# Kernel tuning notes

Hardware: AMD Instinct MI355X
Metric: run time of the kernel (lower is better)

The kernel has to match this reference:

```python
import jax, jax.numpy as jnp
import numpy as np

EPS = 0.0  # GINConv eps

def _gin_conv(x, edge_index, W1, b1, W2, b2, n_nodes):
    # GINConv: mlp((1+eps)*x + sum_{j in N(i)} x_j)
    src, dst = edge_index[0], edge_index[1]
    agg = jax.ops.segment_sum(x[src], dst, num_segments=n_nodes)  # [N, d]
    h = (1.0 + EPS) * x + agg
    h = jax.nn.relu(h @ W1 + b1)  # Linear -> Identity(BN off) -> ReLU
    return h @ W2 + b2            # second Linear


def setup_inputs() -> dict:
    key = jax.random.key(0)
    ks = jax.random.split(key, 10)
    N, E = 50000, 600000
    d_in, d_hid, d_out = 128, 256, 128
    x = jax.random.normal(ks[0], (N, d_in), dtype=jnp.float32)
    edge_index = jax.random.randint(ks[1], (2, E), 0, N, dtype=jnp.int64)

    def lin(k, fan_in, fan_out):
        bound = 1.0 / np.sqrt(fan_in)
        kw, kb = jax.random.split(k)
        W = jax.random.uniform(kw, (fan_in, fan_out), jnp.float32, -bound, bound)
        b = jax.random.uniform(kb, (fan_out,), jnp.float32, -bound, bound)
        return W, b

    W1a, b1a = lin(ks[2], d_in, d_hid)   # conv0 mlp: 128->256
    W2a, b2a = lin(ks[3], d_hid, d_hid)  # conv0 mlp: 256->256
    W1b, b1b = lin(ks[4], d_hid, d_hid)  # conv1 mlp: 256->256
    W2b, b2b = lin(ks[5], d_hid, d_out)  # conv1 mlp: 256->128
    return {"x": x, "W1a": W1a, "b1a": b1a, "W2a": W2a, "b2a": b2a,
            "W1b": W1b, "b1b": b1b, "W2b": W2b, "b2b": b2b,
            "edge_index": edge_index}


def reference(x, W1a, b1a, W2a, b2a, W1b, b1b, W2b, b2b, edge_index):
    n_nodes = x.shape[0]
    # layer 0: GINConv -> relu (use_bn=False; dropout is identity in eval)
    h = _gin_conv(x, edge_index, W1a, b1a, W2a, b2a, n_nodes)
    h = jax.nn.relu(h)
    # final GINConv (no activation after, per forward())
    return _gin_conv(h, edge_index, W1b, b1b, W2b, b2b, n_nodes)
```

## Files before the change

kernel.cpp:

```cpp
#include <hip/hip_runtime.h>


typedef __bf16 bf16x8 __attribute__((ext_vector_type(8)));
typedef float f32x4 __attribute__((ext_vector_type(4)));
typedef float f32x2 __attribute__((ext_vector_type(2)));
typedef unsigned short u16x4 __attribute__((ext_vector_type(4)));
typedef unsigned short u16x8 __attribute__((ext_vector_type(8)));
typedef unsigned int uint32;
typedef uint32 u32x4 __attribute__((ext_vector_type(4)));

__device__ __forceinline__ unsigned short f2bf(float f) {
  uint32 u = __builtin_bit_cast(uint32, f);
  u += 0x7FFFu + ((u >> 16) & 1u);
  return (unsigned short)(u >> 16);
}
__device__ __forceinline__ f32x2 bfpair(uint32 w) {
  f32x2 r;
  r.x = __builtin_bit_cast(float, w << 16);
  r.y = __builtin_bit_cast(float, w & 0xFFFF0000u);
  return r;
}

#define G2L16(gp, lp)                                                        \
  __builtin_amdgcn_global_load_lds(                                          \
      (const __attribute__((address_space(1))) void*)(gp),                   \
      (__attribute__((address_space(3))) void*)(lp), 16, 0, 0)

__global__ void hist(const int* __restrict__ eidx, int* __restrict__ deg, int E) {
  int e = blockIdx.x * blockDim.x + threadIdx.x;
  if (e < E) atomicAdd(&deg[eidx[e + E]], 1);
}

__global__ __launch_bounds__(256) void scan_all(
    const int* __restrict__ deg, int* __restrict__ offs, int* __restrict__ pos,
    int* __restrict__ aggr, int* __restrict__ incl, int* __restrict__ flg,
    int Nn, int nb) {
  __shared__ int sm[256];
  __shared__ int s_prefix;
  const int t = threadIdx.x;
  const int b = blockIdx.x;
  const int i = b * 256 + t;
  int v = (i < Nn) ? deg[i] : 0;
  sm[t] = v;
  __syncthreads();
#pragma unroll
  for (int off = 1; off < 256; off <<= 1) {
    int add = (t >= off) ? sm[t - off] : 0;
    __syncthreads();
    sm[t] += add;
    __syncthreads();
  }
  if (t == 255) {
    atomicExch(&aggr[b], sm[255]);
    atomicExch(&flg[b], 1);
  }
  if (b == 0) {
    for (int j = t; j < nb; j += 256)
      while (atomicAdd(&flg[j], 0) == 0) __builtin_amdgcn_s_sleep(1);
    __syncthreads();
    int a = (t < nb) ? atomicAdd(&aggr[t], 0) : 0;
    __shared__ int sb[256];
    sb[t] = a;
    __syncthreads();
#pragma unroll
    for (int off = 1; off < 256; off <<= 1) {
      int add = (t >= off) ? sb[t - off] : 0;
      __syncthreads();
      sb[t] += add;
      __syncthreads();
    }
    if (t < nb) atomicExch(&incl[t], sb[t]);
    __syncthreads();
    if (t == 0) atomicExch(&flg[nb], 1);
    if (t == 0) s_prefix = 0;
  } else {
    if (t == 0) {
      while (atomicAdd(&flg[nb], 0) == 0) __builtin_amdgcn_s_sleep(8);
      s_prefix = atomicAdd(&incl[b - 1], 0);
    }
  }
  __syncthreads();
  int ex = s_prefix + sm[t] - v;
  if (i < Nn) {
    offs[i] = ex;
    pos[i] = ex;
    if (i == Nn - 1) offs[Nn] = ex + v;
  }
}

__global__ void fill_csr(const int* __restrict__ eidx, int* __restrict__ pos,
                         int* __restrict__ esrc, int E) {
  int e = blockIdx.x * blockDim.x + threadIdx.x;
  if (e < E) {
    int s = eidx[e];
    int d = eidx[e + E];
    int p = atomicAdd(&pos[d], 1);
    esrc[p] = s;
  }
}

__global__ __launch_bounds__(256) void prep(
    int* __restrict__ zp, int zn,
    const float* __restrict__ x, unsigned short* __restrict__ xb, long long n4,
    const float* __restrict__ W1a, const float* __restrict__ W2a,
    const float* __restrict__ W1b, const float* __restrict__ W2b,
    unsigned short* __restrict__ w1t, unsigned short* __restrict__ w2t,
    unsigned short* __restrict__ w3t, unsigned short* __restrict__ w4t) {
  int zb = (zn + 255) >> 8;
  int b = blockIdx.x;
  int t = threadIdx.x;
  if (b < zb) {
    int i = b * 256 + t;
    if (i < zn) zp[i] = 0;
  } else if (b < zb + 768) {
    int i = (b - zb) * 256 + t;
    const float* W;
    unsigned short* WT;
    int K, N, j;
    if (i < 32768) {
      W = W1a; WT = w1t; K = 128; N = 256; j = i;
    } else if (i < 98304) {
      W = W2a; WT = w2t; K = 256; N = 256; j = i - 32768;
    } else if (i < 163840) {
      W = W1b; WT = w3t; K = 256; N = 256; j = i - 98304;
    } else {
      W = W2b; WT = w4t; K = 256; N = 128; j = i - 163840;
    }
    int k = j / N, n = j - k * N;
    WT[n * K + k] = f2bf(W[j]);
  } else {
    long long i = (long long)(b - zb - 768) * 256 + t;
    long long stride = (long long)(gridDim.x - zb - 768) * 256;
    for (; i < n4; i += stride) {
      float4 v = ((const float4*)x)[i];
      u16x4 o;
      o.x = f2bf(v.x); o.y = f2bf(v.y); o.z = f2bf(v.z); o.w = f2bf(v.w);
      ((u16x4*)xb)[i] = o;
    }
  }
}

__global__ __launch_bounds__(256) void agg_bf16_128(
    unsigned short* __restrict__ out, const unsigned short* __restrict__ xb,
    const int* __restrict__ offs, const int* __restrict__ esrc, int Nn) {
  int node = blockIdx.x * 4 + (threadIdx.x >> 6);
  if (node >= Nn) return;
  int lane = threadIdx.x & 63;
  int grp = lane >> 4, l16 = lane & 15;
  int beg = offs[node], end = offs[node + 1];
  int total = end - beg + 1;
  const unsigned short* xp = xb + l16 * 8;
  f32x2 acc[4] = {};
  for (int j0 = 0; j0 < total; j0 += 16) {
#pragma unroll
    for (int u = 0; u < 4; ++u) {
      int j = j0 + u * 4 + grp;
      int rv = esrc[beg + j - (j > 0)];
      long long row = (j > 0 && j < total) ? rv : node;
      float sel = (j < total) ? 1.f : 0.f;
      f32x2 fsel = {sel, sel};
      u32x4 w = *(const u32x4*)(xp + row * 128);
#pragma unroll
      for (int k = 0; k < 4; ++k) acc[k] += bfpair(w[k]) * fsel;
    }
  }
  float s[8];
#pragma unroll
  for (int k = 0; k < 4; ++k) { s[2 * k] = acc[k].x; s[2 * k + 1] = acc[k].y; }
#pragma unroll
  for (int k = 0; k < 8; ++k) s[k] += __shfl_xor(s[k], 16);
#pragma unroll
  for (int k = 0; k < 8; ++k) s[k] += __shfl_xor(s[k], 32);
  if (grp == 0) {
    u16x8 o;
#pragma unroll
    for (int k = 0; k < 8; ++k) o[k] = f2bf(s[k]);
    *(u16x8*)(out + (long long)node * 128 + l16 * 8) = o;
  }
}

__global__ __launch_bounds__(256) void agg_bf16_256(
    unsigned short* __restrict__ out, const unsigned short* __restrict__ h,
    const int* __restrict__ offs, const int* __restrict__ esrc, int Nn) {
  int node = blockIdx.x * 4 + (threadIdx.x >> 6);
  if (node >= Nn) return;
  int lane = threadIdx.x & 63;
  int grp = lane >> 5, l32 = lane & 31;
  int beg = offs[node], end = offs[node + 1];
  int total = end - beg + 1;
  const unsigned short* hp = h + l32 * 8;
  f32x2 acc[4] = {};
  for (int j0 = 0; j0 < total; j0 += 16) {
#pragma unroll
    for (int u = 0; u < 8; ++u) {
      int j = j0 + u * 2 + grp;
      int rv = esrc[beg + j - (j > 0)];
      long long row = (j > 0 && j < total) ? rv : node;
      float sel = (j < total) ? 1.f : 0.f;
      f32x2 fsel = {sel, sel};
      u32x4 w = *(const u32x4*)(hp + row * 256);
#pragma unroll
      for (int k = 0; k < 4; ++k) acc[k] += bfpair(w[k]) * fsel;
    }
  }
  float s[8];
#pragma unroll
  for (int k = 0; k < 4; ++k) { s[2 * k] = acc[k].x; s[2 * k + 1] = acc[k].y; }
#pragma unroll
  for (int k = 0; k < 8; ++k) s[k] += __shfl_xor(s[k], 32);
  if (grp == 0) {
    u16x8 o;
#pragma unroll
    for (int k = 0; k < 8; ++k) o[k] = f2bf(s[k]);
    *(u16x8*)(out + (long long)node * 256 + l32 * 8) = o;
  }
}

template <int K1, int N2, bool OUT_BF16>
__global__ __launch_bounds__(256) void fused_mlp(
    const unsigned short* __restrict__ A,
    const unsigned short* __restrict__ BT1, const float* __restrict__ b1,
    const unsigned short* __restrict__ BT2, const float* __restrict__ b2,
    void* __restrict__ Cout, int M) {
  __shared__ unsigned short As[64 * 32];
  __shared__ unsigned short Bs[256 * 32];
  __shared__ unsigned short Ts[64 * 264];
  const int tid = threadIdx.x;
  const int wave = tid >> 6, lane = tid & 63;
  const int quad = lane >> 4, l16 = lane & 15;
  const int rowBase = blockIdx.x * 64;
  const int r16 = lane >> 2;
  const int kq = lane & 3;

  long long arow = min(rowBase + wave * 16 + r16, M - 1);
  const unsigned short* ga = A + arow * K1 + kq * 8;
  const unsigned short* gb = BT1 + (long long)(wave * 64 + r16) * K1 + kq * 8;
  unsigned short* la = As + wave * 16 * 32;
  f32x4 acc[4][4] = {};
  for (int k0 = 0; k0 < K1; k0 += 32) {
    G2L16(ga, la);
    ga += 32;
#pragma unroll
    for (int c = 0; c < 4; ++c)
      G2L16(gb + (long long)(16 * c) * K1, Bs + (wave * 64 + 16 * c) * 32);
    gb += 32;
    __syncthreads();
    bf16x8 af[4], bfr[4];
#pragma unroll
    for (int mi = 0; mi < 4; ++mi)
      af[mi] = *(const bf16x8*)(As + (mi * 16 + l16) * 32 + quad * 8);
#pragma unroll
    for (int ni = 0; ni < 4; ++ni)
      bfr[ni] = *(const bf16x8*)(Bs + (wave * 64 + ni * 16 + l16) * 32 + quad * 8);
#pragma unroll
    for (int mi = 0; mi < 4; ++mi)
#pragma unroll
      for (int ni = 0; ni < 4; ++ni)
        acc[mi][ni] = __builtin_amdgcn_mfma_f32_16x16x32_bf16(
            af[mi], bfr[ni], acc[mi][ni], 0, 0, 0);
    __syncthreads();
  }
#pragma unroll
  for (int ni = 0; ni < 4; ++ni) {
    int col = wave * 64 + ni * 16 + l16;
    float bv = b1[col];
#pragma unroll
    for (int mi = 0; mi < 4; ++mi)
#pragma unroll
      for (int r = 0; r < 4; ++r) {
        int row = mi * 16 + quad * 4 + r;
        Ts[row * 264 + col] = f2bf(fmaxf(acc[mi][ni][r] + bv, 0.f));
      }
  }
  __syncthreads();

  constexpr int NI2 = N2 / 64;
  const int wcol = wave * (N2 / 4);
  const unsigned short* gb2 = BT2 + (long long)(wcol + r16) * 256 + kq * 8;
  f32x4 acc2[4][NI2] = {};
  for (int k2 = 0; k2 < 256; k2 += 32) {
#pragma unroll
    for (int c = 0; c < NI2; ++c)
      G2L16(gb2 + (long long)(16 * c) * 256, Bs + (wcol + 16 * c) * 32);
    gb2 += 32;
    __syncthreads();
    bf16x8 af[4], bfr[NI2];
#pragma unroll
    for (int mi = 0; mi < 4; ++mi)
      af[mi] = *(const bf16x8*)(Ts + (mi * 16 + l16) * 264 + k2 + quad * 8);
#pragma unroll
    for (int ni = 0; ni < NI2; ++ni)
      bfr[ni] = *(const bf16x8*)(Bs + (wcol + ni * 16 + l16) * 32 + quad * 8);
#pragma unroll
    for (int mi = 0; mi < 4; ++mi)
#pragma unroll
      for (int ni = 0; ni < NI2; ++ni)
        acc2[mi][ni] = __builtin_amdgcn_mfma_f32_16x16x32_bf16(
            af[mi], bfr[ni], acc2[mi][ni], 0, 0, 0);
    __syncthreads();
  }
#pragma unroll
  for (int ni = 0; ni < NI2; ++ni) {
    int col = wcol + ni * 16 + l16;
    float bv = b2[col];
#pragma unroll
    for (int mi = 0; mi < 4; ++mi)
#pragma unroll
      for (int r = 0; r < 4; ++r) {
        int row = rowBase + mi * 16 + quad * 4 + r;
        if (row < M) {
          float o = acc2[mi][ni][r] + bv;
          if (OUT_BF16)
            ((unsigned short*)Cout)[(long long)row * N2 + col] = f2bf(fmaxf(o, 0.f));
          else
            ((float*)Cout)[(long long)row * N2 + col] = o;
        }
      }
  }
}

extern "C" void kernel_launch(void* const* d_in, const int* in_sizes, int n_in,
                              void* d_out, int out_size, void* d_ws, size_t ws_size,
                              hipStream_t stream) {
  const float* x   = (const float*)d_in[0];
  const float* W1a = (const float*)d_in[1];
  const float* b1a = (const float*)d_in[2];
  const float* W2a = (const float*)d_in[3];
  const float* b2a = (const float*)d_in[4];
  const float* W1b = (const float*)d_in[5];
  const float* b1b = (const float*)d_in[6];
  const float* W2b = (const float*)d_in[7];
  const float* b2b = (const float*)d_in[8];
  const int*   ei  = (const int*)d_in[9];

  const int Nn = in_sizes[0] / 128;
  const int E  = in_sizes[9] / 2;
  float* out = (float*)d_out;

  const int nb = (Nn + 255) / 256;

  unsigned short* h   = (unsigned short*)d_ws;
  unsigned short* g0  = h  + (size_t)Nn * 256;
  unsigned short* g1  = g0 + (size_t)Nn * 128;
  unsigned short* xb  = g1 + (size_t)Nn * 256;
  unsigned short* w1t = xb + (size_t)Nn * 128;
  unsigned short* w2t = w1t + 256 * 128;
  unsigned short* w3t = w2t + 256 * 256;
  unsigned short* w4t = w3t + 256 * 256;
  int* deg  = (int*)(w4t + 128 * 256);
  int* flg  = deg + Nn;
  int* aggr = flg + nb + 1;
  int* incl = aggr + nb;
  int* offs = incl + nb;
  int* pos  = offs + Nn + 1;
  int* esrc = pos + Nn;

  dim3 blk(256);
  int zn = Nn + nb + 1;
  int zb = (zn + 255) / 256;

  prep<<<zb + 768 + 2048, blk, 0, stream>>>(deg, zn, x, xb,
                                            (long long)Nn * 128 / 4,
                                            W1a, W2a, W1b, W2b,
                                            w1t, w2t, w3t, w4t);
  hist<<<(E + 255) / 256, blk, 0, stream>>>(ei, deg, E);
  scan_all<<<nb, blk, 0, stream>>>(deg, offs, pos, aggr, incl, flg, Nn, nb);
  fill_csr<<<(E + 255) / 256, blk, 0, stream>>>(ei, pos, esrc, E);

  int aggBlocks = (Nn + 3) / 4;
  int mlpBlocks = (Nn + 63) / 64;

  agg_bf16_128<<<aggBlocks, blk, 0, stream>>>(g0, xb, offs, esrc, Nn);
  fused_mlp<128, 256, true><<<mlpBlocks, blk, 0, stream>>>(
      g0, w1t, b1a, w2t, b2a, h, Nn);
  agg_bf16_256<<<aggBlocks, blk, 0, stream>>>(g1, h, offs, esrc, Nn);
  fused_mlp<256, 128, false><<<mlpBlocks, blk, 0, stream>>>(
      g1, w3t, b1b, w4t, b2b, out, Nn);
}
```

Measured before the change: 293.5 us.

## Load MLP GEMM operands directly from global into registers, dropping LDS staging barriers

The fused two-layer MLP kernel no longer stages A and weight tiles through shared memory with global_load_lds and per-k-step barriers. Each wave now loads its MFMA fragments straight from global memory into registers, leaving only the hidden-activation tile in LDS and one barrier between the two GEMMs. This removes the barrier stalls and LDS traffic in the k-loops and frees LDS, which may allow higher occupancy. In exchange, every wave re-reads the same A rows from global or L2 (four times redundantly), and the per-lane loads use less coalesced access patterns.

```diff
diff --git a/kernel.cpp b/kernel.cpp
--- a/kernel.cpp
+++ b/kernel.cpp
@@ -20,11 +20,6 @@
   r.y = __builtin_bit_cast(float, w & 0xFFFF0000u);
   return r;
 }
-
-#define G2L16(gp, lp)                                                        \
-  __builtin_amdgcn_global_load_lds(                                          \
-      (const __attribute__((address_space(1))) void*)(gp),                   \
-      (__attribute__((address_space(3))) void*)(lp), 16, 0, 0)
 
 __global__ void hist(const int* __restrict__ eidx, int* __restrict__ deg, int E) {
   int e = blockIdx.x * blockDim.x + threadIdx.x;
@@ -217,48 +212,42 @@
 }
 
 template <int K1, int N2, bool OUT_BF16>
-__global__ __launch_bounds__(256) void fused_mlp(
+__global__ __launch_bounds__(256) void mlp_nobar(
     const unsigned short* __restrict__ A,
     const unsigned short* __restrict__ BT1, const float* __restrict__ b1,
     const unsigned short* __restrict__ BT2, const float* __restrict__ b2,
     void* __restrict__ Cout, int M) {
-  __shared__ unsigned short As[64 * 32];
-  __shared__ unsigned short Bs[256 * 32];
-  __shared__ unsigned short Ts[64 * 264];
-  const int tid = threadIdx.x;
-  const int wave = tid >> 6, lane = tid & 63;
+  constexpr int LDT = 264;
+  __shared__ unsigned short Ts[64 * LDT];
+  const int wave = threadIdx.x >> 6, lane = threadIdx.x & 63;
   const int quad = lane >> 4, l16 = lane & 15;
   const int rowBase = blockIdx.x * 64;
-  const int r16 = lane >> 2;
-  const int kq = lane & 3;
-
-  long long arow = min(rowBase + wave * 16 + r16, M - 1);
-  const unsigned short* ga = A + arow * K1 + kq * 8;
-  const unsigned short* gb = BT1 + (long long)(wave * 64 + r16) * K1 + kq * 8;
-  unsigned short* la = As + wave * 16 * 32;
-  f32x4 acc[4][4] = {};
-  for (int k0 = 0; k0 < K1; k0 += 32) {
-    G2L16(ga, la);
-    ga += 32;
-#pragma unroll
-    for (int c = 0; c < 4; ++c)
-      G2L16(gb + (long long)(16 * c) * K1, Bs + (wave * 64 + 16 * c) * 32);
-    gb += 32;
-    __syncthreads();
-    bf16x8 af[4], bfr[4];
-#pragma unroll
-    for (int mi = 0; mi < 4; ++mi)
-      af[mi] = *(const bf16x8*)(As + (mi * 16 + l16) * 32 + quad * 8);
+
+  const unsigned short* aptr[4];
+#pragma unroll
+  for (int mi = 0; mi < 4; ++mi) {
+    long long r = min(rowBase + mi * 16 + l16, M - 1);
+    aptr[mi] = A + r * K1 + quad * 8;
+  }
+  const unsigned short* bptr1 =
+      BT1 + (long long)(wave * 64 + l16) * K1 + quad * 8;
+
+  f32x4 acc1[4][4] = {};
+#pragma unroll 2
+  for (int kk = 0; kk < K1 / 32; ++kk) {
+    bf16x8 af[4], bf[4];
+#pragma unroll
+    for (int mi = 0; mi < 4; ++mi)
+      af[mi] = *(const bf16x8*)(aptr[mi] + kk * 32);
 #pragma unroll
     for (int ni = 0; ni < 4; ++ni)
-      bfr[ni] = *(const bf16x8*)(Bs + (wave * 64 + ni * 16 + l16) * 32 + quad * 8);
+      bf[ni] = *(const bf16x8*)(bptr1 + (long long)ni * 16 * K1 + kk * 32);
 #pragma unroll
     for (int mi = 0; mi < 4; ++mi)
 #pragma unroll
       for (int ni = 0; ni < 4; ++ni)
-        acc[mi][ni] = __builtin_amdgcn_mfma_f32_16x16x32_bf16(
-            af[mi], bfr[ni], acc[mi][ni], 0, 0, 0);
-    __syncthreads();
+        acc1[mi][ni] = __builtin_amdgcn_mfma_f32_16x16x32_bf16(
+            af[mi], bf[ni], acc1[mi][ni], 0, 0, 0);
   }
 #pragma unroll
   for (int ni = 0; ni < 4; ++ni) {
@@ -269,35 +258,31 @@
 #pragma unroll
       for (int r = 0; r < 4; ++r) {
         int row = mi * 16 + quad * 4 + r;
-        Ts[row * 264 + col] = f2bf(fmaxf(acc[mi][ni][r] + bv, 0.f));
+        Ts[row * LDT + col] = f2bf(fmaxf(acc1[mi][ni][r] + bv, 0.f));
       }
   }
   __syncthreads();
 
   constexpr int NI2 = N2 / 64;
   const int wcol = wave * (N2 / 4);
-  const unsigned short* gb2 = BT2 + (long long)(wcol + r16) * 256 + kq * 8;
+  const unsigned short* bptr2 =
+      BT2 + (long long)(wcol + l16) * 256 + quad * 8;
   f32x4 acc2[4][NI2] = {};
-  for (int k2 = 0; k2 < 256; k2 += 32) {
-#pragma unroll
-    for (int c = 0; c < NI2; ++c)
-      G2L16(gb2 + (long long)(16 * c) * 256, Bs + (wcol + 16 * c) * 32);
-    gb2 += 32;
-    __syncthreads();
-    bf16x8 af[4], bfr[NI2];
-#pragma unroll
-    for (int mi = 0; mi < 4; ++mi)
-      af[mi] = *(const bf16x8*)(Ts + (mi * 16 + l16) * 264 + k2 + quad * 8);
+#pragma unroll 2
+  for (int kk = 0; kk < 8; ++kk) {
+    bf16x8 af[4], bf[NI2];
+#pragma unroll
+    for (int mi = 0; mi < 4; ++mi)
+      af[mi] = *(const bf16x8*)(Ts + (mi * 16 + l16) * LDT + kk * 32 + quad * 8);
 #pragma unroll
     for (int ni = 0; ni < NI2; ++ni)
-      bfr[ni] = *(const bf16x8*)(Bs + (wcol + ni * 16 + l16) * 32 + quad * 8);
+      bf[ni] = *(const bf16x8*)(bptr2 + (long long)ni * 16 * 256 + kk * 32);
 #pragma unroll
     for (int mi = 0; mi < 4; ++mi)
 #pragma unroll
       for (int ni = 0; ni < NI2; ++ni)
         acc2[mi][ni] = __builtin_amdgcn_mfma_f32_16x16x32_bf16(
-            af[mi], bfr[ni], acc2[mi][ni], 0, 0, 0);
-    __syncthreads();
+            af[mi], bf[ni], acc2[mi][ni], 0, 0, 0);
   }
 #pragma unroll
   for (int ni = 0; ni < NI2; ++ni) {
@@ -371,9 +356,9 @@
   int mlpBlocks = (Nn + 63) / 64;
 
   agg_bf16_128<<<aggBlocks, blk, 0, stream>>>(g0, xb, offs, esrc, Nn);
-  fused_mlp<128, 256, true><<<mlpBlocks, blk, 0, stream>>>(
+  mlp_nobar<128, 256, true><<<mlpBlocks, blk, 0, stream>>>(
       g0, w1t, b1a, w2t, b2a, h, Nn);
   agg_bf16_256<<<aggBlocks, blk, 0, stream>>>(g1, h, offs, esrc, Nn);
-  fused_mlp<256, 128, false><<<mlpBlocks, blk, 0, stream>>>(
+  mlp_nobar<256, 128, false><<<mlpBlocks, blk, 0, stream>>>(
       g1, w3t, b1b, w4t, b2b, out, Nn);
 }
```

After: 326.1 us. 11.1% more time.
